# Optimization experiments

Hardware: AMD Instinct MI355X
Metric: run time of the kernel (lower is better)

Reference implementation:

```python
import jax, jax.numpy as jnp
import numpy as np

SIZE = 2.0            # scene extent, matches init size
N_LEVELS = 16         # Instant-NGP default
TABLE_SIZE = 1 << 19  # hash entries per level (power of 2)
FEAT = 2              # embedding_length per level
BASE_RES = 16         # init resolution
MAX_RES = 2048
N_POINTS = 1 << 21

_OFFS = np.array([[(c >> d) & 1 for d in range(3)] for c in range(8)])  # [8,3] corner bits
_PRIMES = np.array([1, 2654435761, 805459861], dtype=np.uint32)         # NGP spatial hash primes


def setup_inputs() -> dict:
    key = jax.random.key(0)
    k1, k2 = jax.random.split(key)
    xyz = (jax.random.uniform(k1, (N_POINTS, 3), dtype=jnp.float32) - 0.5) * SIZE
    tables = jax.random.normal(k2, (N_LEVELS, TABLE_SIZE, FEAT), dtype=jnp.float32) * 1e-2
    # geometric resolution schedule 16 -> 2048 over 16 levels
    growth = (MAX_RES / BASE_RES) ** (np.arange(N_LEVELS) / (N_LEVELS - 1))
    resolutions = jnp.asarray(np.floor(BASE_RES * growth).astype(np.int32))
    return {"xyz": xyz, "tables": tables, "resolutions": resolutions}


def _encode(xyz, tables, resolutions):
    u = xyz / SIZE + 0.5                              # [N,3] in [0,1)
    offs_u = jnp.asarray(_OFFS.astype(np.uint32))     # [8,3]
    offs_f = jnp.asarray(_OFFS.astype(np.float32))    # [8,3]
    primes = jnp.asarray(_PRIMES)

    def level(_, xs):
        table, res = xs                               # [T,F], scalar int32
        p = u * res.astype(jnp.float32)               # [N,3]
        p0 = jnp.floor(p)
        w = p - p0                                    # trilinear fractions [N,3]
        c = p0.astype(jnp.uint32)[:, None, :] + offs_u[None]     # [N,8,3]
        h = (c[..., 0] * primes[0]) ^ (c[..., 1] * primes[1]) ^ (c[..., 2] * primes[2])
        idx = (h & jnp.uint32(TABLE_SIZE - 1)).astype(jnp.int32)  # [N,8]
        feats = table[idx]                                        # [N,8,F] gather
        wc = jnp.prod(jnp.where(offs_f[None] > 0, w[:, None, :], 1.0 - w[:, None, :]), axis=-1)  # [N,8]
        return None, jnp.sum(feats * wc[..., None], axis=1)      # [N,F]

    _, embs = jax.lax.scan(level, None, (tables, resolutions))   # [L,N,F]
    n = xyz.shape[0]
    return jnp.transpose(embs, (1, 0, 2)).reshape(n, N_LEVELS * FEAT)


def reference(xyz, tables, resolutions):
    return _encode(xyz, tables, resolutions)
```

## Files before the change

kernel.cpp:

```cpp
#include <hip/hip_runtime.h>
#include <hip/hip_fp16.h>

#define NLV 16
#define TBL (1u << 19)
#define TMASK (TBL - 1u)
#define P1 2654435761u
#define P2 805459861u
#define NBIN (1 << 15)

typedef float vf2 __attribute__((ext_vector_type(2)));
typedef float vf4 __attribute__((ext_vector_type(4)));
typedef unsigned vu2 __attribute__((ext_vector_type(2)));
typedef unsigned vu4 __attribute__((ext_vector_type(4)));
typedef int vi4 __attribute__((ext_vector_type(4)));

__device__ __forceinline__ vf2 h2_to_f2(unsigned bits) {
    union { unsigned u; __half2 h; } c; c.u = bits;
    float2 f = __half22float2(c.h);
    vf2 r; r.x = f.x; r.y = f.y; return r;
}
__device__ __forceinline__ unsigned f2_to_h2(float a, float b) {
    union { __half2 h; unsigned u; } c; c.h = __floats2half2_rn(a, b);
    return c.u;
}

__device__ __forceinline__ unsigned mort5(unsigned v) {
    v &= 31u;
    v = (v | (v << 16)) & 0x030000FFu;
    v = (v | (v << 8))  & 0x0300F00Fu;
    v = (v | (v << 4))  & 0x030C30C3u;
    v = (v | (v << 2))  & 0x09249249u;
    return v;
}

__device__ __forceinline__ unsigned bin_of(float ux, float uy, float uz) {
    unsigned bx = min(31u, (unsigned)(ux * 32.0f));
    unsigned by = min(31u, (unsigned)(uy * 32.0f));
    unsigned bz = min(31u, (unsigned)(uz * 32.0f));
    return mort5(bx) | (mort5(by) << 1) | (mort5(bz) << 2);
}

__global__ __launch_bounds__(256) void convert_and_hist(
    const float* __restrict__ tables, unsigned* __restrict__ htab, int total,
    const float* __restrict__ xyz, unsigned* __restrict__ hist, int n,
    int gridC)
{
    if ((int)blockIdx.x < gridC) {
        int i = blockIdx.x * 256 + threadIdx.x;
        int e0 = i * 2;
        if (e0 >= total) return;
        vf4 v = *(const vf4*)(tables + (size_t)e0 * 2);
        vu2 o; o.x = f2_to_h2(v.x, v.y); o.y = f2_to_h2(v.z, v.w);
        *(vu2*)(htab + e0) = o;
    } else {
        int t = (blockIdx.x - gridC) * 256 + threadIdx.x;
        int p = t * 4;
        if (p >= n) return;
        if (p + 3 < n) {
            vf4 a = *(const vf4*)(xyz + (size_t)p * 3);
            vf4 b = *(const vf4*)(xyz + (size_t)p * 3 + 4);
            vf4 c = *(const vf4*)(xyz + (size_t)p * 3 + 8);
            atomicAdd(&hist[bin_of(a.x*0.5f+0.5f, a.y*0.5f+0.5f, a.z*0.5f+0.5f)], 1u);
            atomicAdd(&hist[bin_of(a.w*0.5f+0.5f, b.x*0.5f+0.5f, b.y*0.5f+0.5f)], 1u);
            atomicAdd(&hist[bin_of(b.z*0.5f+0.5f, b.w*0.5f+0.5f, c.x*0.5f+0.5f)], 1u);
            atomicAdd(&hist[bin_of(c.y*0.5f+0.5f, c.z*0.5f+0.5f, c.w*0.5f+0.5f)], 1u);
        } else {
            for (int q = 0; q < 4 && p + q < n; ++q) {
                float ux = xyz[(size_t)(p+q)*3+0]*0.5f+0.5f;
                float uy = xyz[(size_t)(p+q)*3+1]*0.5f+0.5f;
                float uz = xyz[(size_t)(p+q)*3+2]*0.5f+0.5f;
                atomicAdd(&hist[bin_of(ux,uy,uz)], 1u);
            }
        }
    }
}

__global__ __launch_bounds__(1024) void scan_bins(unsigned* __restrict__ hist)
{
    __shared__ unsigned part[1024];
    int t = threadIdx.x;
    int base = t * (NBIN / 1024);
    unsigned s = 0;
    for (int j = 0; j < NBIN / 1024; ++j) s += hist[base + j];
    part[t] = s;
    __syncthreads();
    for (int off = 1; off < 1024; off <<= 1) {
        unsigned v = (t >= off) ? part[t - off] : 0u;
        __syncthreads();
        part[t] += v;
        __syncthreads();
    }
    unsigned run = (t == 0) ? 0u : part[t - 1];
    for (int j = 0; j < NBIN / 1024; ++j) {
        unsigned tmp = hist[base + j];
        hist[base + j] = run;
        run += tmp;
    }
}

__global__ __launch_bounds__(256) void scatter_kernel(
    const float* __restrict__ xyz, unsigned* __restrict__ start,
    vf4* __restrict__ u4s, int* __restrict__ orig, int n)
{
    int t = blockIdx.x * 256 + threadIdx.x;
    int p = t * 4;
    if (p >= n) return;
    float U[4][3];
    int cnt = (p + 3 < n) ? 4 : (n - p);
    if (cnt == 4) {
        vf4 a = *(const vf4*)(xyz + (size_t)p * 3);
        vf4 b = *(const vf4*)(xyz + (size_t)p * 3 + 4);
        vf4 c = *(const vf4*)(xyz + (size_t)p * 3 + 8);
        U[0][0]=a.x; U[0][1]=a.y; U[0][2]=a.z;
        U[1][0]=a.w; U[1][1]=b.x; U[1][2]=b.y;
        U[2][0]=b.z; U[2][1]=b.w; U[2][2]=c.x;
        U[3][0]=c.y; U[3][1]=c.z; U[3][2]=c.w;
    } else {
        for (int q = 0; q < cnt; ++q) {
            U[q][0]=xyz[(size_t)(p+q)*3+0];
            U[q][1]=xyz[(size_t)(p+q)*3+1];
            U[q][2]=xyz[(size_t)(p+q)*3+2];
        }
    }
#pragma unroll
    for (int q = 0; q < 4; ++q) {
        if (q >= cnt) break;
        float ux = U[q][0]*0.5f+0.5f, uy = U[q][1]*0.5f+0.5f, uz = U[q][2]*0.5f+0.5f;
        unsigned pos = atomicAdd(&start[bin_of(ux,uy,uz)], 1u);
        orig[pos] = p + q;
        vf4 r; r.x = ux; r.y = uy; r.z = uz; r.w = 0.0f;
        u4s[pos] = r;
    }
}

__global__ __launch_bounds__(256) void ngp_gather_s(
    const vf4* __restrict__ u4s,
    const unsigned* __restrict__ htab,
    const int* __restrict__ resolutions,
    unsigned* __restrict__ wsout,
    int n, int nbPerLevel, int Lbase)
{
    int L = Lbase + blockIdx.x / nbPerLevel;
    int chunk = blockIdx.x % nbPerLevel;
    int p0 = chunk * 1024 + (int)threadIdx.x;

    float res = (float)resolutions[L];
    const unsigned* __restrict__ tab = htab + (size_t)L * TBL;
    unsigned* __restrict__ wl = wsout + (size_t)L * n;

    unsigned idx[4][8];
    float wx[4], wyz[4][4];
    bool valid[4];

#pragma unroll
    for (int q = 0; q < 4; ++q) {
        int p = p0 + q * 256;
        valid[q] = (p < n);
        int pp = valid[q] ? p : 0;
        vf4 u = u4s[pp];
        float px = u.x * res, py = u.y * res, pz = u.z * res;
        float fx = floorf(px), fy = floorf(py), fz = floorf(pz);
        float wxl = px - fx, wyl = py - fy, wzl = pz - fz;
        unsigned cx = (unsigned)fx, cy = (unsigned)fy, cz = (unsigned)fz;
        unsigned hx0 = cx, hx1 = cx + 1u;
        unsigned hy0 = cy * P1, hy1 = hy0 + P1;
        unsigned hz0 = cz * P2, hz1 = hz0 + P2;
#pragma unroll
        for (int c = 0; c < 8; ++c)
            idx[q][c] = ((((c & 1) ? hx1 : hx0) ^
                          ((c & 2) ? hy1 : hy0) ^
                          ((c & 4) ? hz1 : hz0)) & TMASK);
        float vy = 1.0f - wyl, vz = 1.0f - wzl;
        wx[q] = wxl;
        wyz[q][0] = vy * vz;  wyz[q][1] = wyl * vz;
        wyz[q][2] = vy * wzl; wyz[q][3] = wyl * wzl;
    }

    unsigned d[4][8];
#pragma unroll
    for (int q = 0; q < 4; ++q)
#pragma unroll
        for (int c = 0; c < 8; ++c)
            d[q][c] = tab[idx[q][c]];

#pragma unroll
    for (int q = 0; q < 4; ++q) {
        float vx = 1.0f - wx[q];
        float a0 = 0.0f, a1 = 0.0f;
#pragma unroll
        for (int c = 0; c < 8; ++c) {
            float w = wyz[q][c >> 1] * ((c & 1) ? wx[q] : vx);
            vf2 f = h2_to_f2(d[q][c]);
            a0 += f.x * w;
            a1 += f.y * w;
        }
        int p = p0 + q * 256;
        if (valid[q]) wl[p] = f2_to_h2(a0, a1);
    }
}

__global__ __launch_bounds__(256) void ngp_finalize_s(
    const unsigned* __restrict__ ws, const int* __restrict__ orig,
    float* __restrict__ out, int n)
{
    int t = blockIdx.x * 256 + threadIdx.x;
    int i = t * 4;
    if (i >= n) return;

    if (i + 3 < n && (n & 3) == 0) {
        vu4 m[NLV];
#pragma unroll
        for (int L = 0; L < NLV; ++L)
            m[L] = *(const vu4*)(ws + (size_t)L * n + i);
        vi4 og = *(const vi4*)(orig + i);
#pragma unroll
        for (int pt = 0; pt < 4; ++pt) {
            int op = pt == 0 ? og.x : pt == 1 ? og.y : pt == 2 ? og.z : og.w;
            vf4* o = (vf4*)(out + (size_t)op * (NLV * 2));
#pragma unroll
            for (int j = 0; j < 8; ++j) {
                unsigned ba = pt == 0 ? m[2 * j].x : pt == 1 ? m[2 * j].y
                             : pt == 2 ? m[2 * j].z : m[2 * j].w;
                unsigned bb = pt == 0 ? m[2 * j + 1].x : pt == 1 ? m[2 * j + 1].y
                             : pt == 2 ? m[2 * j + 1].z : m[2 * j + 1].w;
                vf2 ga = h2_to_f2(ba), gb = h2_to_f2(bb);
                vf4 r; r.x = ga.x; r.y = ga.y; r.z = gb.x; r.w = gb.y;
                o[j] = r;
            }
        }
    } else {
        for (int pt = 0; pt < 4 && i + pt < n; ++pt) {
            int op = orig[i + pt];
            vf4* o = (vf4*)(out + (size_t)op * (NLV * 2));
#pragma unroll
            for (int j = 0; j < 8; ++j) {
                vf2 ga = h2_to_f2(ws[(size_t)(2 * j) * n + i + pt]);
                vf2 gb = h2_to_f2(ws[(size_t)(2 * j + 1) * n + i + pt]);
                vf4 r; r.x = ga.x; r.y = ga.y; r.z = gb.x; r.w = gb.y;
                o[j] = r;
            }
        }
    }
}

__global__ __launch_bounds__(256) void ngp_encode_kernel(
    const float* __restrict__ xyz,
    const float* __restrict__ tables,
    const int* __restrict__ resolutions,
    float* __restrict__ out,
    int n)
{
    int p = blockIdx.x * blockDim.x + threadIdx.x;
    if (p >= n) return;

    float x = xyz[(size_t)p * 3 + 0];
    float y = xyz[(size_t)p * 3 + 1];
    float z = xyz[(size_t)p * 3 + 2];
    float ux = x * 0.5f + 0.5f;
    float uy = y * 0.5f + 0.5f;
    float uz = z * 0.5f + 0.5f;

    float acc[NLV * 2];

#pragma unroll
    for (int L = 0; L < NLV; ++L) {
        float res = (float)resolutions[L];
        float px = ux * res, py = uy * res, pz = uz * res;
        float fx = floorf(px), fy = floorf(py), fz = floorf(pz);
        float wx = px - fx, wy = py - fy, wz = pz - fz;
        unsigned cx = (unsigned)fx, cy = (unsigned)fy, cz = (unsigned)fz;
        unsigned hx0 = cx, hx1 = cx + 1u;
        unsigned hy0 = cy * P1, hy1 = hy0 + P1;
        unsigned hz0 = cz * P2, hz1 = hz0 + P2;
        const vf2* __restrict__ tab = (const vf2*)tables + (size_t)L * TBL;
        float vx = 1.0f - wx, vy = 1.0f - wy, vz = 1.0f - wz;
        float a0 = 0.0f, a1 = 0.0f;
#pragma unroll
        for (int c = 0; c < 8; ++c) {
            unsigned h = ((c & 1) ? hx1 : hx0) ^
                         ((c & 2) ? hy1 : hy0) ^
                         ((c & 4) ? hz1 : hz0);
            vf2 f = tab[h & TMASK];
            float w = ((c & 1) ? wx : vx) *
                      ((c & 2) ? wy : vy) *
                      ((c & 4) ? wz : vz);
            a0 += f.x * w;
            a1 += f.y * w;
        }
        acc[L * 2 + 0] = a0;
        acc[L * 2 + 1] = a1;
    }

    vf4* o = (vf4*)(out + (size_t)p * (NLV * 2));
#pragma unroll
    for (int i = 0; i < 8; ++i) {
        vf4 r; r.x = acc[i * 4 + 0]; r.y = acc[i * 4 + 1];
        r.z = acc[i * 4 + 2]; r.w = acc[i * 4 + 3];
        o[i] = r;
    }
}

extern "C" void kernel_launch(void* const* d_in, const int* in_sizes, int n_in,
                              void* d_out, int out_size, void* d_ws, size_t ws_size,
                              hipStream_t stream) {
    const float* xyz = (const float*)d_in[0];
    const float* tables = (const float*)d_in[1];
    const int* resolutions = (const int*)d_in[2];
    float* out = (float*)d_out;

    int n = in_sizes[0] / 3;
    const int totalEntries = NLV * (int)TBL;

    const size_t tabBytes  = (size_t)totalEntries * 4;
    const size_t u4Bytes   = (size_t)n * sizeof(vf4);
    const size_t origBytes = (size_t)n * 4;
    const size_t histBytes = (size_t)NBIN * 4;
    const size_t wsoutBytes = (size_t)NLV * (size_t)n * 4;
    const size_t need = tabBytes + u4Bytes + origBytes + histBytes + wsoutBytes;

    if (ws_size >= need) {
        char* base = (char*)d_ws;
        unsigned* htab  = (unsigned*)base;                       base += tabBytes;
        vf4*      u4s   = (vf4*)base;                            base += u4Bytes;
        int*      orig  = (int*)base;                            base += origBytes;
        unsigned* hist  = (unsigned*)base;                       base += histBytes;
        unsigned* wsout = (unsigned*)base;

        hipMemsetAsync(hist, 0, histBytes, stream);

        int gridC = (totalEntries / 2 + 255) / 256;
        int grid4 = ((n + 3) / 4 + 255) / 256;
        hipLaunchKernelGGL(convert_and_hist, dim3(gridC + grid4), dim3(256), 0,
                           stream, tables, htab, totalEntries, xyz, hist, n, gridC);

        hipLaunchKernelGGL(scan_bins, dim3(1), dim3(1024), 0, stream, hist);
        hipLaunchKernelGGL(scatter_kernel, dim3(grid4), dim3(256), 0, stream,
                           xyz, hist, u4s, orig, n);

        int nbPerLevel = (n + 1023) / 1024;
        int gridHalf = 8 * nbPerLevel;
        hipLaunchKernelGGL(ngp_gather_s, dim3(gridHalf), dim3(256), 0, stream,
                           u4s, htab, resolutions, wsout, n, nbPerLevel, 0);
        hipLaunchKernelGGL(ngp_gather_s, dim3(gridHalf), dim3(256), 0, stream,
                           u4s, htab, resolutions, wsout, n, nbPerLevel, 8);

        int gridF = ((n + 3) / 4 + 255) / 256;
        hipLaunchKernelGGL(ngp_finalize_s, dim3(gridF), dim3(256), 0, stream,
                           wsout, orig, out, n);
    } else {
        int grid = (n + 255) / 256;
        hipLaunchKernelGGL(ngp_encode_kernel, dim3(grid), dim3(256), 0, stream,
                           xyz, tables, resolutions, out, n);
    }
}
```

Before: 811.2 us.

## Fuse all encoding stages into one cooperative persistent kernel with grid syncs

Replaces the six-launch pipeline (memset, convert+hist, scan, scatter, two gather halves, finalize) with a single cooperative kernel of 1024 blocks. It uses grid-wide syncs between the table conversion, histogram, single-block scan, scatter, per-level gather and finalize phases, and loops over work items. The aim is to remove launch gaps and tail effects between stages. In exchange, the scan runs in one block while the other blocks wait, grid.sync has its own cost, and the fixed grid size may cap occupancy for the gather phase. If the cooperative launch fails, it falls back to the multi-kernel path with the gather merged into one launch.

```diff
diff --git a/kernel.cpp b/kernel.cpp
--- a/kernel.cpp
+++ b/kernel.cpp
@@ -1,5 +1,8 @@
 #include <hip/hip_runtime.h>
+#include <hip/hip_cooperative_groups.h>
 #include <hip/hip_fp16.h>
+
+namespace cg = cooperative_groups;
 
 #define NLV 16
 #define TBL (1u << 19)
@@ -7,6 +10,7 @@
 #define P1 2654435761u
 #define P2 805459861u
 #define NBIN (1 << 15)
+#define NBLK 1024
 
 typedef float vf2 __attribute__((ext_vector_type(2)));
 typedef float vf4 __attribute__((ext_vector_type(4)));
@@ -38,6 +42,210 @@
     unsigned by = min(31u, (unsigned)(uy * 32.0f));
     unsigned bz = min(31u, (unsigned)(uz * 32.0f));
     return mort5(bx) | (mort5(by) << 1) | (mort5(bz) << 2);
+}
+
+__global__ __launch_bounds__(256) void ngp_mega(
+    const float* __restrict__ xyz,
+    const float* __restrict__ tables,
+    const int* __restrict__ resolutions,
+    unsigned* __restrict__ htab,
+    vf4* __restrict__ u4s,
+    int* __restrict__ orig,
+    unsigned* __restrict__ hist,
+    unsigned* __restrict__ wsout,
+    float* __restrict__ out,
+    int n, int totalEntries)
+{
+    cg::grid_group grid = cg::this_grid();
+    const int NB = (int)gridDim.x;
+    const int NT = NB * 256;
+    const int tid = (int)blockIdx.x * 256 + (int)threadIdx.x;
+
+    for (int i = tid; i < NBIN; i += NT) hist[i] = 0u;
+    for (int i = tid; i < totalEntries / 2; i += NT) {
+        int e0 = i * 2;
+        vf4 v = *(const vf4*)(tables + (size_t)e0 * 2);
+        vu2 o; o.x = f2_to_h2(v.x, v.y); o.y = f2_to_h2(v.z, v.w);
+        *(vu2*)(htab + e0) = o;
+    }
+    grid.sync();
+
+    for (int t = tid; t * 4 < n; t += NT) {
+        int p = t * 4;
+        if (p + 3 < n) {
+            vf4 a = *(const vf4*)(xyz + (size_t)p * 3);
+            vf4 b = *(const vf4*)(xyz + (size_t)p * 3 + 4);
+            vf4 c = *(const vf4*)(xyz + (size_t)p * 3 + 8);
+            atomicAdd(&hist[bin_of(a.x*0.5f+0.5f, a.y*0.5f+0.5f, a.z*0.5f+0.5f)], 1u);
+            atomicAdd(&hist[bin_of(a.w*0.5f+0.5f, b.x*0.5f+0.5f, b.y*0.5f+0.5f)], 1u);
+            atomicAdd(&hist[bin_of(b.z*0.5f+0.5f, b.w*0.5f+0.5f, c.x*0.5f+0.5f)], 1u);
+            atomicAdd(&hist[bin_of(c.y*0.5f+0.5f, c.z*0.5f+0.5f, c.w*0.5f+0.5f)], 1u);
+        } else {
+            for (int q = 0; q < 4 && p + q < n; ++q) {
+                float ux = xyz[(size_t)(p+q)*3+0]*0.5f+0.5f;
+                float uy = xyz[(size_t)(p+q)*3+1]*0.5f+0.5f;
+                float uz = xyz[(size_t)(p+q)*3+2]*0.5f+0.5f;
+                atomicAdd(&hist[bin_of(ux,uy,uz)], 1u);
+            }
+        }
+    }
+    grid.sync();
+
+    if (blockIdx.x == 0) {
+        __shared__ unsigned part[256];
+        int t = (int)threadIdx.x;
+        int base = t * (NBIN / 256);
+        unsigned s = 0;
+        for (int j = 0; j < NBIN / 256; ++j) s += hist[base + j];
+        part[t] = s;
+        __syncthreads();
+        for (int off = 1; off < 256; off <<= 1) {
+            unsigned v = (t >= off) ? part[t - off] : 0u;
+            __syncthreads();
+            part[t] += v;
+            __syncthreads();
+        }
+        unsigned run = (t == 0) ? 0u : part[t - 1];
+        for (int j = 0; j < NBIN / 256; ++j) {
+            unsigned tmp = hist[base + j];
+            hist[base + j] = run;
+            run += tmp;
+        }
+    }
+    grid.sync();
+
+    for (int t = tid; t * 4 < n; t += NT) {
+        int p = t * 4;
+        float U[4][3];
+        int cnt = (p + 3 < n) ? 4 : (n - p);
+        if (cnt == 4) {
+            vf4 a = *(const vf4*)(xyz + (size_t)p * 3);
+            vf4 b = *(const vf4*)(xyz + (size_t)p * 3 + 4);
+            vf4 c = *(const vf4*)(xyz + (size_t)p * 3 + 8);
+            U[0][0]=a.x; U[0][1]=a.y; U[0][2]=a.z;
+            U[1][0]=a.w; U[1][1]=b.x; U[1][2]=b.y;
+            U[2][0]=b.z; U[2][1]=b.w; U[2][2]=c.x;
+            U[3][0]=c.y; U[3][1]=c.z; U[3][2]=c.w;
+        } else {
+            for (int q = 0; q < cnt; ++q) {
+                U[q][0]=xyz[(size_t)(p+q)*3+0];
+                U[q][1]=xyz[(size_t)(p+q)*3+1];
+                U[q][2]=xyz[(size_t)(p+q)*3+2];
+            }
+        }
+#pragma unroll
+        for (int q = 0; q < 4; ++q) {
+            if (q >= cnt) break;
+            float ux = U[q][0]*0.5f+0.5f, uy = U[q][1]*0.5f+0.5f, uz = U[q][2]*0.5f+0.5f;
+            unsigned pos = atomicAdd(&hist[bin_of(ux,uy,uz)], 1u);
+            orig[pos] = p + q;
+            vf4 r; r.x = ux; r.y = uy; r.z = uz; r.w = 0.0f;
+            u4s[pos] = r;
+        }
+    }
+    grid.sync();
+
+    {
+        int nbPerLevel = (n + 1023) / 1024;
+        for (int item = (int)blockIdx.x; item < NLV * nbPerLevel; item += NB) {
+            int L = item / nbPerLevel;
+            int chunk = item % nbPerLevel;
+            int p0 = chunk * 1024 + (int)threadIdx.x;
+
+            float res = (float)resolutions[L];
+            const unsigned* __restrict__ tab = htab + (size_t)L * TBL;
+            unsigned* __restrict__ wl = wsout + (size_t)L * n;
+
+            unsigned idx[4][8];
+            float wx[4], wyz[4][4];
+            bool valid[4];
+
+#pragma unroll
+            for (int q = 0; q < 4; ++q) {
+                int p = p0 + q * 256;
+                valid[q] = (p < n);
+                int pp = valid[q] ? p : 0;
+                vf4 u = u4s[pp];
+                float px = u.x * res, py = u.y * res, pz = u.z * res;
+                float fx = floorf(px), fy = floorf(py), fz = floorf(pz);
+                float wxl = px - fx, wyl = py - fy, wzl = pz - fz;
+                unsigned cx = (unsigned)fx, cy = (unsigned)fy, cz = (unsigned)fz;
+                unsigned hx0 = cx, hx1 = cx + 1u;
+                unsigned hy0 = cy * P1, hy1 = hy0 + P1;
+                unsigned hz0 = cz * P2, hz1 = hz0 + P2;
+#pragma unroll
+                for (int c = 0; c < 8; ++c)
+                    idx[q][c] = ((((c & 1) ? hx1 : hx0) ^
+                                  ((c & 2) ? hy1 : hy0) ^
+                                  ((c & 4) ? hz1 : hz0)) & TMASK);
+                float vy = 1.0f - wyl, vz = 1.0f - wzl;
+                wx[q] = wxl;
+                wyz[q][0] = vy * vz;  wyz[q][1] = wyl * vz;
+                wyz[q][2] = vy * wzl; wyz[q][3] = wyl * wzl;
+            }
+
+            unsigned d[4][8];
+#pragma unroll
+            for (int q = 0; q < 4; ++q)
+#pragma unroll
+                for (int c = 0; c < 8; ++c)
+                    d[q][c] = tab[idx[q][c]];
+
+#pragma unroll
+            for (int q = 0; q < 4; ++q) {
+                float vx = 1.0f - wx[q];
+                float a0 = 0.0f, a1 = 0.0f;
+#pragma unroll
+                for (int c = 0; c < 8; ++c) {
+                    float w = wyz[q][c >> 1] * ((c & 1) ? wx[q] : vx);
+                    vf2 f = h2_to_f2(d[q][c]);
+                    a0 += f.x * w;
+                    a1 += f.y * w;
+                }
+                int p = p0 + q * 256;
+                if (valid[q]) wl[p] = f2_to_h2(a0, a1);
+            }
+        }
+    }
+    grid.sync();
+
+    for (int t = tid; t * 4 < n; t += NT) {
+        int i = t * 4;
+        if (i + 3 < n) {
+            vu4 m[NLV];
+#pragma unroll
+            for (int L = 0; L < NLV; ++L)
+                m[L] = *(const vu4*)(wsout + (size_t)L * n + i);
+            vi4 og = *(const vi4*)(orig + i);
+#pragma unroll
+            for (int pt = 0; pt < 4; ++pt) {
+                int op = pt == 0 ? og.x : pt == 1 ? og.y : pt == 2 ? og.z : og.w;
+                vf4* o = (vf4*)(out + (size_t)op * (NLV * 2));
+#pragma unroll
+                for (int j = 0; j < 8; ++j) {
+                    unsigned ba = pt == 0 ? m[2 * j].x : pt == 1 ? m[2 * j].y
+                                 : pt == 2 ? m[2 * j].z : m[2 * j].w;
+                    unsigned bb = pt == 0 ? m[2 * j + 1].x : pt == 1 ? m[2 * j + 1].y
+                                 : pt == 2 ? m[2 * j + 1].z : m[2 * j + 1].w;
+                    vf2 ga = h2_to_f2(ba), gb = h2_to_f2(bb);
+                    vf4 r; r.x = ga.x; r.y = ga.y; r.z = gb.x; r.w = gb.y;
+                    o[j] = r;
+                }
+            }
+        } else {
+            for (int pt = 0; pt < 4 && i + pt < n; ++pt) {
+                int op = orig[i + pt];
+                vf4* o = (vf4*)(out + (size_t)op * (NLV * 2));
+#pragma unroll
+                for (int j = 0; j < 8; ++j) {
+                    vf2 ga = h2_to_f2(wsout[(size_t)(2 * j) * n + i + pt]);
+                    vf2 gb = h2_to_f2(wsout[(size_t)(2 * j + 1) * n + i + pt]);
+                    vf4 r; r.x = ga.x; r.y = ga.y; r.z = gb.x; r.w = gb.y;
+                    o[j] = r;
+                }
+            }
+        }
+    }
 }
 
 __global__ __launch_bounds__(256) void convert_and_hist(
@@ -138,9 +346,9 @@
     const unsigned* __restrict__ htab,
     const int* __restrict__ resolutions,
     unsigned* __restrict__ wsout,
-    int n, int nbPerLevel, int Lbase)
-{
-    int L = Lbase + blockIdx.x / nbPerLevel;
+    int n, int nbPerLevel)
+{
+    int L = blockIdx.x / nbPerLevel;
     int chunk = blockIdx.x % nbPerLevel;
     int p0 = chunk * 1024 + (int)threadIdx.x;
 
@@ -309,7 +517,7 @@
     float* out = (float*)d_out;
 
     int n = in_sizes[0] / 3;
-    const int totalEntries = NLV * (int)TBL;
+    int totalEntries = NLV * (int)TBL;
 
     const size_t tabBytes  = (size_t)totalEntries * 4;
     const size_t u4Bytes   = (size_t)n * sizeof(vf4);
@@ -326,27 +534,31 @@
         unsigned* hist  = (unsigned*)base;                       base += histBytes;
         unsigned* wsout = (unsigned*)base;
 
-        hipMemsetAsync(hist, 0, histBytes, stream);
-
-        int gridC = (totalEntries / 2 + 255) / 256;
-        int grid4 = ((n + 3) / 4 + 255) / 256;
-        hipLaunchKernelGGL(convert_and_hist, dim3(gridC + grid4), dim3(256), 0,
-                           stream, tables, htab, totalEntries, xyz, hist, n, gridC);
-
-        hipLaunchKernelGGL(scan_bins, dim3(1), dim3(1024), 0, stream, hist);
-        hipLaunchKernelGGL(scatter_kernel, dim3(grid4), dim3(256), 0, stream,
-                           xyz, hist, u4s, orig, n);
-
-        int nbPerLevel = (n + 1023) / 1024;
-        int gridHalf = 8 * nbPerLevel;
-        hipLaunchKernelGGL(ngp_gather_s, dim3(gridHalf), dim3(256), 0, stream,
-                           u4s, htab, resolutions, wsout, n, nbPerLevel, 0);
-        hipLaunchKernelGGL(ngp_gather_s, dim3(gridHalf), dim3(256), 0, stream,
-                           u4s, htab, resolutions, wsout, n, nbPerLevel, 8);
-
-        int gridF = ((n + 3) / 4 + 255) / 256;
-        hipLaunchKernelGGL(ngp_finalize_s, dim3(gridF), dim3(256), 0, stream,
-                           wsout, orig, out, n);
+        void* args[] = {
+            (void*)&xyz, (void*)&tables, (void*)&resolutions,
+            (void*)&htab, (void*)&u4s, (void*)&orig, (void*)&hist,
+            (void*)&wsout, (void*)&out, (void*)&n, (void*)&totalEntries
+        };
+        hipError_t e = hipLaunchCooperativeKernel(
+            (const void*)ngp_mega, dim3(NBLK), dim3(256), args, 0, stream);
+
+        if (e != hipSuccess) {
+            hipMemsetAsync(hist, 0, histBytes, stream);
+            int gridC = (totalEntries / 2 + 255) / 256;
+            int grid4 = ((n + 3) / 4 + 255) / 256;
+            hipLaunchKernelGGL(convert_and_hist, dim3(gridC + grid4), dim3(256),
+                               0, stream, tables, htab, totalEntries, xyz, hist,
+                               n, gridC);
+            hipLaunchKernelGGL(scan_bins, dim3(1), dim3(1024), 0, stream, hist);
+            hipLaunchKernelGGL(scatter_kernel, dim3(grid4), dim3(256), 0, stream,
+                               xyz, hist, u4s, orig, n);
+            int nbPerLevel = (n + 1023) / 1024;
+            hipLaunchKernelGGL(ngp_gather_s, dim3(NLV * nbPerLevel), dim3(256),
+                               0, stream, u4s, htab, resolutions, wsout, n,
+                               nbPerLevel);
+            hipLaunchKernelGGL(ngp_finalize_s, dim3(grid4), dim3(256), 0, stream,
+                               wsout, orig, out, n);
+        }
     } else {
         int grid = (n + 255) / 256;
         hipLaunchKernelGGL(ngp_encode_kernel, dim3(grid), dim3(256), 0, stream,
```

Result: slower. 1.442 ms (+77.7%).
